# Kernel tuning notes

Measured on AMD Instinct MI355X. Metric: run time of the kernel, lower is better.

Reference implementation:

```python
import jax, jax.numpy as jnp
import numpy as np

N = 65536   # base nodes
M = 65536   # union local nodes
E = 1048576 # base edges
EL = 1048576 # local edges
K = 131072  # membership entries
F = 128     # in_channels
H = 128     # hidden_dim
L = 2       # num_layers
OUT = 2
ALPHA = 0.9


def setup_inputs() -> dict:
    key = jax.random.key(0)
    ks = jax.random.split(key, 16)
    s = 1.0 / np.sqrt(H)
    return {
        "x": jax.random.normal(ks[0], (N, F), jnp.float32),
        "edge_index": jax.random.randint(ks[1], (2, E), 0, N, jnp.int64 if jax.config.jax_enable_x64 else jnp.int32),
        "edge_weight": jax.random.uniform(ks[2], (E,), jnp.float32),
        "local_x0": jax.random.normal(ks[3], (M, F), jnp.float32),
        "copy2orig": jax.random.randint(ks[4], (M,), 0, N),
        "local_adj_index": jax.random.randint(ks[5], (2, EL), 0, M),
        "local_adj_value": jax.random.uniform(ks[6], (EL,), jnp.float32),
        "memb_idx": jax.random.randint(ks[7], (K,), 0, M),
        "memb_gid": jax.random.randint(ks[8], (K,), 0, 64),
        "B": 64,
        "Wb_in": jax.random.normal(ks[9], (F, H), jnp.float32) * s,
        "bb_in": jnp.zeros((H,), jnp.float32),
        "Wl_in": jax.random.normal(ks[10], (F, H), jnp.float32) * s,
        "bl_in": jnp.zeros((H,), jnp.float32),
        "W_base": jax.random.normal(ks[11], (L, H, H), jnp.float32) * s,
        "b_base": jnp.zeros((L, H), jnp.float32),
        "W_local": jax.random.normal(ks[12], (L, H, H), jnp.float32) * s,
        "b_local": jnp.zeros((L, H), jnp.float32),
        "Wp": jax.random.normal(ks[13], (H, OUT), jnp.float32) * s,
        "bp": jnp.zeros((OUT,), jnp.float32),
    }


def reference(x, edge_index, edge_weight, local_x0, copy2orig, local_adj_index,
              local_adj_value, memb_idx, memb_gid, B, Wb_in, bb_in, Wl_in, bl_in,
              W_base, b_base, W_local, b_local, Wp, bp):
    n = x.shape[0]
    m = local_x0.shape[0]
    # input projections (dropout is identity in eval mode)
    base_x = jax.nn.relu(x @ Wb_in + bb_in)
    local_x = jax.nn.relu(local_x0 @ Wl_in + bl_in)
    src, dst = edge_index[0], edge_index[1]
    lsrc, ldst = local_adj_index[0], local_adj_index[1]
    for l in range(W_base.shape[0]):
        # base graph propagation: normalized-adjacency spmm then linear+relu
        base_agg = jax.ops.segment_sum(base_x[src] * edge_weight[:, None], dst, num_segments=n)
        base_x = jax.nn.relu(base_agg @ W_base[l] + b_base[l])
        # local union-graph propagation + alpha-mix with base features via copy2orig
        local_agg = jax.ops.segment_sum(local_x[lsrc] * local_adj_value[:, None], ldst, num_segments=m)
        mix = ALPHA * local_agg + (1.0 - ALPHA) * base_x[copy2orig]
        local_x = jax.nn.relu(mix @ W_local[l] + b_local[l])
    # scatter-mean pooling by membership (fused sum + count)
    sub = jax.ops.segment_sum(local_x[memb_idx], memb_gid, num_segments=B)
    cnt = jax.ops.segment_sum(jnp.ones((memb_gid.shape[0], 1), local_x.dtype), memb_gid, num_segments=B)
    sub = sub / jnp.maximum(cnt, 1.0)
    return sub @ Wp + bp
```

## Files before the change

kernel.cpp:

```cpp
#include <hip/hip_runtime.h>

typedef __attribute__((ext_vector_type(8))) short bfrag;
typedef __attribute__((ext_vector_type(4))) float ffrag;

__device__ __forceinline__ ushort f2bf(float f) {
    union { float f; unsigned u; } v{f};
    unsigned r = v.u + 0x7fff + ((v.u >> 16) & 1);
    return (ushort)(r >> 16);
}
__device__ __forceinline__ float bf2f(ushort u) {
    union { unsigned u; float f; } v{(unsigned)u << 16};
    return v.f;
}
__device__ __forceinline__ float bflo(unsigned u) {
    union { unsigned u; float f; } v{u << 16};
    return v.f;
}
__device__ __forceinline__ float bfhi(unsigned u) {
    union { unsigned u; float f; } v{u & 0xffff0000u};
    return v.f;
}


__global__ __launch_bounds__(256) void zero_kernel(int* __restrict__ p, int n) {
    int i = blockIdx.x * 256 + threadIdx.x;
    if (i < n) p[i] = 0;
}


__global__ __launch_bounds__(256) void bhist(const int* __restrict__ dst, int* __restrict__ bcount) {
    __shared__ int h[256];
    const int t = threadIdx.x;
    h[t] = 0;
    __syncthreads();
    const int base = blockIdx.x * 4096;
#pragma unroll
    for (int u = 0; u < 16; ++u)
        atomicAdd(&h[((unsigned)dst[base + u * 256 + t]) >> 8], 1);
    __syncthreads();
    atomicAdd(&bcount[t], h[t]);
}

__global__ __launch_bounds__(256) void bscan(const int* __restrict__ bcount, int* __restrict__ bstart,
                                             int* __restrict__ bcursor) {
    __shared__ int s[256];
    const int t = threadIdx.x;
    int c = bcount[t];
    s[t] = c;
    __syncthreads();
    for (int o = 1; o < 256; o <<= 1) {
        int add = (t >= o) ? s[t - o] : 0;
        __syncthreads();
        s[t] += add;
        __syncthreads();
    }
    int excl = s[t] - c;
    bstart[t] = excl;
    bcursor[t] = excl;
    if (t == 255) bstart[256] = s[t];
}

#define CH 4096

__global__ __launch_bounds__(256) void bucket1(const int* __restrict__ src, const int* __restrict__ dst,
                                               const float* __restrict__ w, int* __restrict__ bcursor,
                                               int2* __restrict__ staged) {
    __shared__ int cnt_s[256], base_l[256], base_g[256], cur[256];
    __shared__ int2 stage[CH];
    __shared__ unsigned char bb[CH];
    const int t = threadIdx.x;
    const int base = blockIdx.x * CH;
    cnt_s[t] = 0;
    __syncthreads();
#pragma unroll
    for (int u = 0; u < CH / 256; ++u) {
        int b = ((unsigned)dst[base + u * 256 + t]) >> 8;
        atomicAdd(&cnt_s[b], 1);
    }
    __syncthreads();
    int v = cnt_s[t];
    base_l[t] = v;
    __syncthreads();
    for (int o = 1; o < 256; o <<= 1) {
        int add = (t >= o) ? base_l[t - o] : 0;
        __syncthreads();
        base_l[t] += add;
        __syncthreads();
    }
    int excl = base_l[t] - v;
    base_l[t] = excl;
    cur[t] = excl;
    base_g[t] = atomicAdd(&bcursor[t], v);
    __syncthreads();
#pragma unroll
    for (int u = 0; u < CH / 256; ++u) {
        int e = base + u * 256 + t;
        int d = dst[e];
        int b = ((unsigned)d) >> 8;
        int p = atomicAdd(&cur[b], 1);
        stage[p] = make_int2((src[e] & 0xffff) | ((d & 255) << 16), __float_as_int(w[e]));
        bb[p] = (unsigned char)b;
    }
    __syncthreads();
    for (int i = t; i < CH; i += 256) {
        int b = bb[i];
        staged[base_g[b] + (i - base_l[b])] = stage[i];
    }
}

__global__ __launch_bounds__(256) void bucket2n(const int* __restrict__ bstart, const int2* __restrict__ staged,
                                                int* __restrict__ start, int2* __restrict__ edges) {
    __shared__ int cnt[256], excl[256], cur[256];
    const int t = threadIdx.x;
    const int b = blockIdx.x;
    cnt[t] = 0;
    __syncthreads();
    const int s0 = bstart[b];
    const int s1 = bstart[b + 1];
    for (int i = s0 + t; i < s1; i += 256) {
        int dl = (staged[i].x >> 16) & 0xff;
        atomicAdd(&cnt[dl], 1);
    }
    __syncthreads();
    int v = cnt[t];
    excl[t] = v;
    __syncthreads();
    for (int o = 1; o < 256; o <<= 1) {
        int add = (t >= o) ? excl[t - o] : 0;
        __syncthreads();
        excl[t] += add;
        __syncthreads();
    }
    int e = excl[t] - v;
    cur[t] = e;
    start[b * 256 + t] = s0 + e;
    if (b == 255 && t == 255) start[256 * 256] = s1;
    __syncthreads();
    for (int i = s0 + t; i < s1; i += 256) {
        int2 se = staged[i];
        int dl = (se.x >> 16) & 0xff;
        int p = s0 + atomicAdd(&cur[dl], 1);
        edges[p] = make_int2(se.x & 0xffff, se.y);
    }
}


__global__ __launch_bounds__(256) void wprep(const float* __restrict__ Wb_in, const float* __restrict__ Wl_in,
                                             const float* __restrict__ W_base, const float* __restrict__ W_local,
                                             ushort* __restrict__ out) {
    int idx = blockIdx.x * 256 + threadIdx.x;
    int mat = idx >> 14;
    int i = idx & 16383;
    int nn = i >> 7, kk = i & 127;
    const float* src;
    switch (mat) {
        case 0: src = Wb_in; break;
        case 1: src = Wl_in; break;
        case 2: src = W_base; break;
        case 3: src = W_base + 16384; break;
        case 4: src = W_local; break;
        default: src = W_local + 16384; break;
    }
    out[(size_t)mat * 16384 + i] = f2bf(src[kk * 128 + nn]);
}


#define ASTRIDE 136

template <bool A_F32, bool MIX>
__global__ __launch_bounds__(256) void gemm_mfma(const void* __restrict__ Ap, const ushort* __restrict__ A2,
                                                 const int* __restrict__ ridx,
                                                 const ushort* __restrict__ Wt, const float* __restrict__ bias,
                                                 ushort* __restrict__ Y) {
    __shared__ ushort As[64 * ASTRIDE];
    __shared__ ushort Bs[128 * ASTRIDE];
    const int tid = threadIdx.x;
    const int r0 = blockIdx.x * 64;

    if (A_F32) {
        const float* A = (const float*)Ap;
#pragma unroll
        for (int p = 0; p < 8; ++p) {
            int c = p * 256 + tid;
            int row = c >> 5, o4 = (c & 31) * 4;
            float4 v = *(const float4*)(A + (size_t)(r0 + row) * 128 + o4);
            ushort4 u;
            u.x = f2bf(v.x); u.y = f2bf(v.y); u.z = f2bf(v.z); u.w = f2bf(v.w);
            *(ushort4*)&As[row * ASTRIDE + o4] = u;
        }
    } else {
        const ushort* A = (const ushort*)Ap;
#pragma unroll
        for (int p = 0; p < 4; ++p) {
            int c = p * 256 + tid;
            int row = c >> 4, o8 = (c & 15) * 8;
            uint4 v = *(const uint4*)(A + (size_t)(r0 + row) * 128 + o8);
            if (MIX) {
                int rr = ridx[r0 + row];
                uint4 v2 = *(const uint4*)(A2 + (size_t)rr * 128 + o8);
                uint4 o;
                float x0, x1;
                x0 = 0.9f * bflo(v.x) + 0.1f * bflo(v2.x);
                x1 = 0.9f * bfhi(v.x) + 0.1f * bfhi(v2.x);
                o.x = (unsigned)f2bf(x0) | ((unsigned)f2bf(x1) << 16);
                x0 = 0.9f * bflo(v.y) + 0.1f * bflo(v2.y);
                x1 = 0.9f * bfhi(v.y) + 0.1f * bfhi(v2.y);
                o.y = (unsigned)f2bf(x0) | ((unsigned)f2bf(x1) << 16);
                x0 = 0.9f * bflo(v.z) + 0.1f * bflo(v2.z);
                x1 = 0.9f * bfhi(v.z) + 0.1f * bfhi(v2.z);
                o.z = (unsigned)f2bf(x0) | ((unsigned)f2bf(x1) << 16);
                x0 = 0.9f * bflo(v.w) + 0.1f * bflo(v2.w);
                x1 = 0.9f * bfhi(v.w) + 0.1f * bfhi(v2.w);
                o.w = (unsigned)f2bf(x0) | ((unsigned)f2bf(x1) << 16);
                v = o;
            }
            *(uint4*)&As[row * ASTRIDE + o8] = v;
        }
    }
#pragma unroll
    for (int p = 0; p < 8; ++p) {
        int c = p * 256 + tid;
        int n = c >> 4, o8 = (c & 15) * 8;
        *(uint4*)&Bs[n * ASTRIDE + o8] = *(const uint4*)(Wt + n * 128 + o8);
    }
    __syncthreads();

    const int lane = tid & 63;
    const int w = tid >> 6;
    const int wm = (w & 1) * 32;
    const int wn = (w >> 1) * 64;
    const int q = lane >> 4;
    const int l16 = lane & 15;

    ffrag acc[2][4];
#pragma unroll
    for (int mt = 0; mt < 2; ++mt)
#pragma unroll
        for (int nt = 0; nt < 4; ++nt) acc[mt][nt] = (ffrag){0.f, 0.f, 0.f, 0.f};

#pragma unroll
    for (int kc = 0; kc < 4; ++kc) {
        bfrag a[2], b[4];
#pragma unroll
        for (int mt = 0; mt < 2; ++mt)
            a[mt] = *(const bfrag*)&As[(wm + mt * 16 + l16) * ASTRIDE + kc * 32 + q * 8];
#pragma unroll
        for (int nt = 0; nt < 4; ++nt)
            b[nt] = *(const bfrag*)&Bs[(wn + nt * 16 + l16) * ASTRIDE + kc * 32 + q * 8];
#pragma unroll
        for (int mt = 0; mt < 2; ++mt)
#pragma unroll
            for (int nt = 0; nt < 4; ++nt)
                acc[mt][nt] = __builtin_amdgcn_mfma_f32_16x16x32_bf16(a[mt], b[nt], acc[mt][nt], 0, 0, 0);
    }

    float bias_v[4];
#pragma unroll
    for (int nt = 0; nt < 4; ++nt) bias_v[nt] = bias[wn + nt * 16 + l16];
#pragma unroll
    for (int mt = 0; mt < 2; ++mt)
#pragma unroll
        for (int nt = 0; nt < 4; ++nt)
#pragma unroll
            for (int r = 0; r < 4; ++r) {
                int row = r0 + wm + mt * 16 + q * 4 + r;
                int col = wn + nt * 16 + l16;
                float v = fmaxf(acc[mt][nt][r] + bias_v[nt], 0.f);
                Y[(size_t)row * 128 + col] = f2bf(v);
            }
}


__global__ __launch_bounds__(256) void spmm_bf16(const int* __restrict__ start, const int2* __restrict__ edges,
                                                 const ushort* __restrict__ X, ushort* __restrict__ Y, int n) {
    int node = (blockIdx.x * 256 + threadIdx.x) >> 5;
    int lane = threadIdx.x & 31;
    if (node >= n) return;
    int s0 = start[node];
    int s1 = start[node + 1];
    const int f = lane * 4;
    float a0 = 0.f, a1 = 0.f, a2 = 0.f, a3 = 0.f;
    int e = s0;
    for (; e + 4 <= s1; e += 4) {
        int2 e0 = edges[e + 0], e1 = edges[e + 1], e2 = edges[e + 2], e3 = edges[e + 3];
        float w0 = __int_as_float(e0.y), w1 = __int_as_float(e1.y);
        float w2 = __int_as_float(e2.y), w3 = __int_as_float(e3.y);
        ushort4 v0 = *(const ushort4*)(X + (size_t)e0.x * 128 + f);
        ushort4 v1 = *(const ushort4*)(X + (size_t)e1.x * 128 + f);
        ushort4 v2 = *(const ushort4*)(X + (size_t)e2.x * 128 + f);
        ushort4 v3 = *(const ushort4*)(X + (size_t)e3.x * 128 + f);
        a0 += w0 * bf2f(v0.x) + w1 * bf2f(v1.x) + w2 * bf2f(v2.x) + w3 * bf2f(v3.x);
        a1 += w0 * bf2f(v0.y) + w1 * bf2f(v1.y) + w2 * bf2f(v2.y) + w3 * bf2f(v3.y);
        a2 += w0 * bf2f(v0.z) + w1 * bf2f(v1.z) + w2 * bf2f(v2.z) + w3 * bf2f(v3.z);
        a3 += w0 * bf2f(v0.w) + w1 * bf2f(v1.w) + w2 * bf2f(v2.w) + w3 * bf2f(v3.w);
    }
    for (; e < s1; ++e) {
        int2 ee = edges[e];
        float w = __int_as_float(ee.y);
        ushort4 v = *(const ushort4*)(X + (size_t)ee.x * 128 + f);
        a0 += w * bf2f(v.x);
        a1 += w * bf2f(v.y);
        a2 += w * bf2f(v.z);
        a3 += w * bf2f(v.w);
    }
    ushort4 o;
    o.x = f2bf(a0);
    o.y = f2bf(a1);
    o.z = f2bf(a2);
    o.w = f2bf(a3);
    *(ushort4*)(Y + (size_t)node * 128 + f) = o;
}


__global__ __launch_bounds__(256) void pool_hist(const int* __restrict__ memb_gid, int* __restrict__ gcount) {
    __shared__ int h[64];
    int t = threadIdx.x;
    if (t < 64) h[t] = 0;
    __syncthreads();
    int base = blockIdx.x * 1024;
#pragma unroll
    for (int u = 0; u < 4; ++u) atomicAdd(&h[memb_gid[base + u * 256 + t]], 1);
    __syncthreads();
    if (t < 64) atomicAdd(&gcount[t], h[t]);
}

__global__ __launch_bounds__(64) void pool_scan(const int* __restrict__ gcount, int* __restrict__ gstart,
                                                int* __restrict__ cursor) {
    __shared__ int s[64];
    int t = threadIdx.x;
    int c = gcount[t];
    s[t] = c;
    __syncthreads();
    int acc = 0;
    for (int j = 0; j < 64; ++j)
        if (j < t) acc += s[j];
    gstart[t] = acc;
    cursor[t] = acc;
    if (t == 63) gstart[64] = acc + c;
}

__global__ __launch_bounds__(256) void pool_scatter(const int* __restrict__ memb_idx,
                                                    const int* __restrict__ memb_gid,
                                                    int* __restrict__ cursor, int* __restrict__ sorted_idx) {
    __shared__ int lhist[64];
    __shared__ int lbase[64];
    __shared__ int loff[1024];
    int t = threadIdx.x;
    if (t < 64) lhist[t] = 0;
    __syncthreads();
    int base = blockIdx.x * 1024;
    int g[4], ix[4];
#pragma unroll
    for (int u = 0; u < 4; ++u) {
        int e = base + u * 256 + t;
        g[u] = memb_gid[e];
        ix[u] = memb_idx[e];
        loff[u * 256 + t] = atomicAdd(&lhist[g[u]], 1);
    }
    __syncthreads();
    if (t < 64) lbase[t] = atomicAdd(&cursor[t], lhist[t]);
    __syncthreads();
#pragma unroll
    for (int u = 0; u < 4; ++u) {
        int pos = lbase[g[u]] + loff[u * 256 + t];
        sorted_idx[pos] = ix[u];
    }
}

__global__ __launch_bounds__(256) void pool_accum(const int* __restrict__ gstart, const int* __restrict__ sorted_idx,
                                                  const ushort* __restrict__ X, float* __restrict__ gsum) {
    const int g = blockIdx.x >> 5;
    const int sgm = blockIdx.x & 31;
    const int gs = gstart[g];
    const int cnt = gstart[g + 1] - gs;
    const int e_begin = gs + ((cnt * sgm) >> 5);
    const int e_end = gs + ((cnt * (sgm + 1)) >> 5);
    const int t = threadIdx.x;
    const int fp = t & 63;
    const int sub = t >> 6;
    float ax = 0.f, ay = 0.f;
#pragma unroll 4
    for (int e = e_begin + sub; e < e_end; e += 4) {
        int idx = sorted_idx[e];
        ushort2 u = *(const ushort2*)(X + (size_t)idx * 128 + fp * 2);
        ax += bf2f(u.x);
        ay += bf2f(u.y);
    }
    __shared__ float sx[256], sy[256];
    sx[t] = ax;
    sy[t] = ay;
    __syncthreads();
    if (t < 64) {
        atomicAdd(&gsum[g * 128 + fp * 2 + 0], sx[t] + sx[t + 64] + sx[t + 128] + sx[t + 192]);
        atomicAdd(&gsum[g * 128 + fp * 2 + 1], sy[t] + sy[t + 64] + sy[t + 128] + sy[t + 192]);
    }
}


__global__ __launch_bounds__(128) void final_kernel(const float* __restrict__ gsum, const int* __restrict__ gcnt,
                                                    const float* __restrict__ Wp, const float* __restrict__ bp,
                                                    float* __restrict__ out) {
    int t = threadIdx.x;
    int g = t >> 1;
    int o = t & 1;
    float inv = 1.f / fmaxf((float)gcnt[g], 1.f);
    float acc = bp[o];
    for (int f = 0; f < 128; ++f) acc += gsum[g * 128 + f] * inv * Wp[f * 2 + o];
    out[g * 2 + o] = acc;
}


extern "C" void kernel_launch(void* const* d_in, const int* in_sizes, int n_in,
                              void* d_out, int out_size, void* d_ws, size_t ws_size,
                              hipStream_t stream) {
    const float* x              = (const float*)d_in[0];
    const int*   edge_index     = (const int*)d_in[1];
    const float* edge_weight    = (const float*)d_in[2];
    const float* local_x0       = (const float*)d_in[3];
    const int*   copy2orig      = (const int*)d_in[4];
    const int*   local_adj_idx  = (const int*)d_in[5];
    const float* local_adj_val  = (const float*)d_in[6];
    const int*   memb_idx       = (const int*)d_in[7];
    const int*   memb_gid       = (const int*)d_in[8];
    const float* Wb_in          = (const float*)d_in[10];
    const float* bb_in          = (const float*)d_in[11];
    const float* Wl_in          = (const float*)d_in[12];
    const float* bl_in          = (const float*)d_in[13];
    const float* W_base         = (const float*)d_in[14];
    const float* b_base         = (const float*)d_in[15];
    const float* W_local        = (const float*)d_in[16];
    const float* b_local        = (const float*)d_in[17];
    const float* Wp             = (const float*)d_in[18];
    const float* bp             = (const float*)d_in[19];
    float* out = (float*)d_out;

    constexpr int N = 65536, M = 65536, E = 1048576, EL = 1048576, K = 131072, H = 128;

    char* wsb = (char*)d_ws;
    size_t off = 0;
    auto alloc = [&](size_t bytes) -> char* {
        char* p = wsb + off;
        off += (bytes + 255) & ~(size_t)255;
        return p;
    };
    int*    bs_start = (int*)alloc((size_t)(N + 1) * 4);
    int2*   bs_edges = (int2*)alloc((size_t)E * 8);
    int2*   bs_stage = (int2*)alloc((size_t)E * 8);
    int*    bs_bcnt  = (int*)alloc(256 * 4);
    int*    bs_bsta  = (int*)alloc(257 * 4);
    int*    bs_bcur  = (int*)alloc(256 * 4);
    int*    ls_start = (int*)alloc((size_t)(M + 1) * 4);
    int2*   ls_edges = (int2*)alloc((size_t)EL * 8);
    int2*   ls_stage = (int2*)alloc((size_t)EL * 8);
    int*    ls_bcnt  = (int*)alloc(256 * 4);
    int*    ls_bsta  = (int*)alloc(257 * 4);
    int*    ls_bcur  = (int*)alloc(256 * 4);
    ushort* bufA     = (ushort*)alloc((size_t)N * H * 2);
    ushort* bufB     = (ushort*)alloc((size_t)M * H * 2);
    ushort* bufC     = (ushort*)alloc((size_t)N * H * 2);
    ushort* bufD     = (ushort*)alloc((size_t)M * H * 2);
    ushort* wt       = (ushort*)alloc((size_t)6 * 16384 * 2);
    int*    p_gcnt   = (int*)alloc(64 * 4);
    int*    p_gstart = (int*)alloc(65 * 4);
    int*    p_cursor = (int*)alloc(64 * 4);
    int*    p_sorted = (int*)alloc((size_t)K * 4);
    float*  pool_sum = (float*)alloc(64 * 128 * 4);

    const int* b_src = edge_index;
    const int* b_dst = edge_index + E;
    const int* l_src = local_adj_idx;
    const int* l_dst = local_adj_idx + EL;

    zero_kernel<<<1, 256, 0, stream>>>(bs_bcnt, 256);
    zero_kernel<<<1, 256, 0, stream>>>(ls_bcnt, 256);
    zero_kernel<<<1, 256, 0, stream>>>(p_gcnt, 64);
    zero_kernel<<<32, 256, 0, stream>>>((int*)pool_sum, 64 * 128);

    wprep<<<384, 256, 0, stream>>>(Wb_in, Wl_in, W_base, W_local, wt);

    bhist<<<E / 4096, 256, 0, stream>>>(b_dst, bs_bcnt);
    bscan<<<1, 256, 0, stream>>>(bs_bcnt, bs_bsta, bs_bcur);
    bucket1<<<E / CH, 256, 0, stream>>>(b_src, b_dst, edge_weight, bs_bcur, bs_stage);
    bucket2n<<<256, 256, 0, stream>>>(bs_bsta, bs_stage, bs_start, bs_edges);

    bhist<<<EL / 4096, 256, 0, stream>>>(l_dst, ls_bcnt);
    bscan<<<1, 256, 0, stream>>>(ls_bcnt, ls_bsta, ls_bcur);
    bucket1<<<EL / CH, 256, 0, stream>>>(l_src, l_dst, local_adj_val, ls_bcur, ls_stage);
    bucket2n<<<256, 256, 0, stream>>>(ls_bsta, ls_stage, ls_start, ls_edges);

    pool_hist<<<K / 1024, 256, 0, stream>>>(memb_gid, p_gcnt);
    pool_scan<<<1, 64, 0, stream>>>(p_gcnt, p_gstart, p_cursor);
    pool_scatter<<<K / 1024, 256, 0, stream>>>(memb_idx, memb_gid, p_cursor, p_sorted);

    gemm_mfma<true, false><<<N / 64, 256, 0, stream>>>(x, nullptr, nullptr, wt, bb_in, bufA);
    gemm_mfma<true, false><<<M / 64, 256, 0, stream>>>(local_x0, nullptr, nullptr, wt + 16384, bl_in, bufB);

    for (int l = 0; l < 2; ++l) {
        spmm_bf16<<<N * 32 / 256, 256, 0, stream>>>(bs_start, bs_edges, bufA, bufC, N);
        spmm_bf16<<<M * 32 / 256, 256, 0, stream>>>(ls_start, ls_edges, bufB, bufD, M);
        gemm_mfma<false, false><<<N / 64, 256, 0, stream>>>(bufC, nullptr, nullptr,
                                                            wt + (size_t)(2 + l) * 16384, b_base + (size_t)l * H, bufA);
        gemm_mfma<false, true><<<M / 64, 256, 0, stream>>>(bufD, bufA, copy2orig,
                                                           wt + (size_t)(4 + l) * 16384, b_local + (size_t)l * H, bufB);
    }

    pool_accum<<<64 * 32, 256, 0, stream>>>(p_gstart, p_sorted, bufB, pool_sum);
    final_kernel<<<1, 128, 0, stream>>>(pool_sum, p_gcnt, Wp, bp, out);
}
```

Baseline: 481.6 us.

## Fuse SpMM aggregation and alpha-mix into the MFMA GEMM prologue

Each SpMM is merged with the following linear layer: a block of 64 nodes aggregates its neighbours straight into shared memory, applies the alpha-mix with the base features in fp32, and then runs the MFMA GEMM. This removes the bufC/bufD round trip through global memory and half the kernel launches. Weight fragments are now read directly from global memory instead of being staged in shared memory, which cuts LDS use and raises occupancy but may cost L2 bandwidth. The mix is now applied before bf16 rounding, which changes numerics slightly.

Result: slower. 528.6 us (+9.8%).

```diff
diff --git a/kernel.cpp b/kernel.cpp
--- a/kernel.cpp
+++ b/kernel.cpp
@@ -10,14 +10,6 @@
 }
 __device__ __forceinline__ float bf2f(ushort u) {
     union { unsigned u; float f; } v{(unsigned)u << 16};
-    return v.f;
-}
-__device__ __forceinline__ float bflo(unsigned u) {
-    union { unsigned u; float f; } v{u << 16};
-    return v.f;
-}
-__device__ __forceinline__ float bfhi(unsigned u) {
-    union { unsigned u; float f; } v{u & 0xffff0000u};
     return v.f;
 }
 
@@ -164,64 +156,23 @@
     out[(size_t)mat * 16384 + i] = f2bf(src[kk * 128 + nn]);
 }
 
-
 #define ASTRIDE 136
 
-template <bool A_F32, bool MIX>
-__global__ __launch_bounds__(256) void gemm_mfma(const void* __restrict__ Ap, const ushort* __restrict__ A2,
-                                                 const int* __restrict__ ridx,
-                                                 const ushort* __restrict__ Wt, const float* __restrict__ bias,
-                                                 ushort* __restrict__ Y) {
+
+__global__ __launch_bounds__(256) void gemm_in(const float* __restrict__ A, const ushort* __restrict__ Wt,
+                                               const float* __restrict__ bias, ushort* __restrict__ Y) {
     __shared__ ushort As[64 * ASTRIDE];
-    __shared__ ushort Bs[128 * ASTRIDE];
     const int tid = threadIdx.x;
     const int r0 = blockIdx.x * 64;
 
-    if (A_F32) {
-        const float* A = (const float*)Ap;
-#pragma unroll
-        for (int p = 0; p < 8; ++p) {
-            int c = p * 256 + tid;
-            int row = c >> 5, o4 = (c & 31) * 4;
-            float4 v = *(const float4*)(A + (size_t)(r0 + row) * 128 + o4);
-            ushort4 u;
-            u.x = f2bf(v.x); u.y = f2bf(v.y); u.z = f2bf(v.z); u.w = f2bf(v.w);
-            *(ushort4*)&As[row * ASTRIDE + o4] = u;
-        }
-    } else {
-        const ushort* A = (const ushort*)Ap;
-#pragma unroll
-        for (int p = 0; p < 4; ++p) {
-            int c = p * 256 + tid;
-            int row = c >> 4, o8 = (c & 15) * 8;
-            uint4 v = *(const uint4*)(A + (size_t)(r0 + row) * 128 + o8);
-            if (MIX) {
-                int rr = ridx[r0 + row];
-                uint4 v2 = *(const uint4*)(A2 + (size_t)rr * 128 + o8);
-                uint4 o;
-                float x0, x1;
-                x0 = 0.9f * bflo(v.x) + 0.1f * bflo(v2.x);
-                x1 = 0.9f * bfhi(v.x) + 0.1f * bfhi(v2.x);
-                o.x = (unsigned)f2bf(x0) | ((unsigned)f2bf(x1) << 16);
-                x0 = 0.9f * bflo(v.y) + 0.1f * bflo(v2.y);
-                x1 = 0.9f * bfhi(v.y) + 0.1f * bfhi(v2.y);
-                o.y = (unsigned)f2bf(x0) | ((unsigned)f2bf(x1) << 16);
-                x0 = 0.9f * bflo(v.z) + 0.1f * bflo(v2.z);
-                x1 = 0.9f * bfhi(v.z) + 0.1f * bfhi(v2.z);
-                o.z = (unsigned)f2bf(x0) | ((unsigned)f2bf(x1) << 16);
-                x0 = 0.9f * bflo(v.w) + 0.1f * bflo(v2.w);
-                x1 = 0.9f * bfhi(v.w) + 0.1f * bfhi(v2.w);
-                o.w = (unsigned)f2bf(x0) | ((unsigned)f2bf(x1) << 16);
-                v = o;
-            }
-            *(uint4*)&As[row * ASTRIDE + o8] = v;
-        }
-    }
 #pragma unroll
     for (int p = 0; p < 8; ++p) {
         int c = p * 256 + tid;
-        int n = c >> 4, o8 = (c & 15) * 8;
-        *(uint4*)&Bs[n * ASTRIDE + o8] = *(const uint4*)(Wt + n * 128 + o8);
+        int row = c >> 5, o4 = (c & 31) * 4;
+        float4 v = *(const float4*)(A + (size_t)(r0 + row) * 128 + o4);
+        ushort4 u;
+        u.x = f2bf(v.x); u.y = f2bf(v.y); u.z = f2bf(v.z); u.w = f2bf(v.w);
+        *(ushort4*)&As[row * ASTRIDE + o4] = u;
     }
     __syncthreads();
 
@@ -246,7 +197,7 @@
             a[mt] = *(const bfrag*)&As[(wm + mt * 16 + l16) * ASTRIDE + kc * 32 + q * 8];
 #pragma unroll
         for (int nt = 0; nt < 4; ++nt)
-            b[nt] = *(const bfrag*)&Bs[(wn + nt * 16 + l16) * ASTRIDE + kc * 32 + q * 8];
+            b[nt] = *(const bfrag*)(Wt + (wn + nt * 16 + l16) * 128 + kc * 32 + q * 8);
 #pragma unroll
         for (int mt = 0; mt < 2; ++mt)
 #pragma unroll
@@ -271,44 +222,108 @@
 }
 
 
-__global__ __launch_bounds__(256) void spmm_bf16(const int* __restrict__ start, const int2* __restrict__ edges,
-                                                 const ushort* __restrict__ X, ushort* __restrict__ Y, int n) {
-    int node = (blockIdx.x * 256 + threadIdx.x) >> 5;
-    int lane = threadIdx.x & 31;
-    if (node >= n) return;
-    int s0 = start[node];
-    int s1 = start[node + 1];
+template <bool MIX>
+__global__ __launch_bounds__(256) void spmm_gemm(const int* __restrict__ start, const int2* __restrict__ edges,
+                                                 const ushort* __restrict__ X, const ushort* __restrict__ A2,
+                                                 const int* __restrict__ ridx, const ushort* __restrict__ Wt,
+                                                 const float* __restrict__ bias, ushort* __restrict__ Y) {
+    __shared__ ushort As[64 * ASTRIDE];
+    const int tid = threadIdx.x;
+    const int r0 = blockIdx.x * 64;
+    const int sw = tid >> 5;
+    const int lane = tid & 31;
     const int f = lane * 4;
-    float a0 = 0.f, a1 = 0.f, a2 = 0.f, a3 = 0.f;
-    int e = s0;
-    for (; e + 4 <= s1; e += 4) {
-        int2 e0 = edges[e + 0], e1 = edges[e + 1], e2 = edges[e + 2], e3 = edges[e + 3];
-        float w0 = __int_as_float(e0.y), w1 = __int_as_float(e1.y);
-        float w2 = __int_as_float(e2.y), w3 = __int_as_float(e3.y);
-        ushort4 v0 = *(const ushort4*)(X + (size_t)e0.x * 128 + f);
-        ushort4 v1 = *(const ushort4*)(X + (size_t)e1.x * 128 + f);
-        ushort4 v2 = *(const ushort4*)(X + (size_t)e2.x * 128 + f);
-        ushort4 v3 = *(const ushort4*)(X + (size_t)e3.x * 128 + f);
-        a0 += w0 * bf2f(v0.x) + w1 * bf2f(v1.x) + w2 * bf2f(v2.x) + w3 * bf2f(v3.x);
-        a1 += w0 * bf2f(v0.y) + w1 * bf2f(v1.y) + w2 * bf2f(v2.y) + w3 * bf2f(v3.y);
-        a2 += w0 * bf2f(v0.z) + w1 * bf2f(v1.z) + w2 * bf2f(v2.z) + w3 * bf2f(v3.z);
-        a3 += w0 * bf2f(v0.w) + w1 * bf2f(v1.w) + w2 * bf2f(v2.w) + w3 * bf2f(v3.w);
-    }
-    for (; e < s1; ++e) {
-        int2 ee = edges[e];
-        float w = __int_as_float(ee.y);
-        ushort4 v = *(const ushort4*)(X + (size_t)ee.x * 128 + f);
-        a0 += w * bf2f(v.x);
-        a1 += w * bf2f(v.y);
-        a2 += w * bf2f(v.z);
-        a3 += w * bf2f(v.w);
-    }
-    ushort4 o;
-    o.x = f2bf(a0);
-    o.y = f2bf(a1);
-    o.z = f2bf(a2);
-    o.w = f2bf(a3);
-    *(ushort4*)(Y + (size_t)node * 128 + f) = o;
+
+#pragma unroll
+    for (int i = 0; i < 8; ++i) {
+        const int node = r0 + i * 8 + sw;
+        const int rl = i * 8 + sw;
+        int s0 = start[node];
+        int s1 = start[node + 1];
+        float a0 = 0.f, a1 = 0.f, a2 = 0.f, a3 = 0.f;
+        int e = s0;
+        for (; e + 4 <= s1; e += 4) {
+            int2 e0 = edges[e + 0], e1 = edges[e + 1], e2 = edges[e + 2], e3 = edges[e + 3];
+            float w0 = __int_as_float(e0.y), w1 = __int_as_float(e1.y);
+            float w2 = __int_as_float(e2.y), w3 = __int_as_float(e3.y);
+            ushort4 v0 = *(const ushort4*)(X + (size_t)e0.x * 128 + f);
+            ushort4 v1 = *(const ushort4*)(X + (size_t)e1.x * 128 + f);
+            ushort4 v2 = *(const ushort4*)(X + (size_t)e2.x * 128 + f);
+            ushort4 v3 = *(const ushort4*)(X + (size_t)e3.x * 128 + f);
+            a0 += w0 * bf2f(v0.x) + w1 * bf2f(v1.x) + w2 * bf2f(v2.x) + w3 * bf2f(v3.x);
+            a1 += w0 * bf2f(v0.y) + w1 * bf2f(v1.y) + w2 * bf2f(v2.y) + w3 * bf2f(v3.y);
+            a2 += w0 * bf2f(v0.z) + w1 * bf2f(v1.z) + w2 * bf2f(v2.z) + w3 * bf2f(v3.z);
+            a3 += w0 * bf2f(v0.w) + w1 * bf2f(v1.w) + w2 * bf2f(v2.w) + w3 * bf2f(v3.w);
+        }
+        for (; e < s1; ++e) {
+            int2 ee = edges[e];
+            float w = __int_as_float(ee.y);
+            ushort4 v = *(const ushort4*)(X + (size_t)ee.x * 128 + f);
+            a0 += w * bf2f(v.x);
+            a1 += w * bf2f(v.y);
+            a2 += w * bf2f(v.z);
+            a3 += w * bf2f(v.w);
+        }
+        if (MIX) {
+            int rr = ridx[node];
+            ushort4 m = *(const ushort4*)(A2 + (size_t)rr * 128 + f);
+            a0 = 0.9f * a0 + 0.1f * bf2f(m.x);
+            a1 = 0.9f * a1 + 0.1f * bf2f(m.y);
+            a2 = 0.9f * a2 + 0.1f * bf2f(m.z);
+            a3 = 0.9f * a3 + 0.1f * bf2f(m.w);
+        }
+        ushort4 o;
+        o.x = f2bf(a0);
+        o.y = f2bf(a1);
+        o.z = f2bf(a2);
+        o.w = f2bf(a3);
+        *(ushort4*)&As[rl * ASTRIDE + f] = o;
+    }
+    __syncthreads();
+
+    const int wlane = tid & 63;
+    const int w = tid >> 6;
+    const int wm = (w & 1) * 32;
+    const int wn = (w >> 1) * 64;
+    const int q = wlane >> 4;
+    const int l16 = wlane & 15;
+
+    ffrag acc[2][4];
+#pragma unroll
+    for (int mt = 0; mt < 2; ++mt)
+#pragma unroll
+        for (int nt = 0; nt < 4; ++nt) acc[mt][nt] = (ffrag){0.f, 0.f, 0.f, 0.f};
+
+#pragma unroll
+    for (int kc = 0; kc < 4; ++kc) {
+        bfrag a[2], b[4];
+#pragma unroll
+        for (int mt = 0; mt < 2; ++mt)
+            a[mt] = *(const bfrag*)&As[(wm + mt * 16 + l16) * ASTRIDE + kc * 32 + q * 8];
+#pragma unroll
+        for (int nt = 0; nt < 4; ++nt)
+            b[nt] = *(const bfrag*)(Wt + (wn + nt * 16 + l16) * 128 + kc * 32 + q * 8);
+#pragma unroll
+        for (int mt = 0; mt < 2; ++mt)
+#pragma unroll
+            for (int nt = 0; nt < 4; ++nt)
+                acc[mt][nt] = __builtin_amdgcn_mfma_f32_16x16x32_bf16(a[mt], b[nt], acc[mt][nt], 0, 0, 0);
+    }
+
+    float bias_v[4];
+#pragma unroll
+    for (int nt = 0; nt < 4; ++nt) bias_v[nt] = bias[wn + nt * 16 + l16];
+#pragma unroll
+    for (int mt = 0; mt < 2; ++mt)
+#pragma unroll
+        for (int nt = 0; nt < 4; ++nt)
+#pragma unroll
+            for (int r = 0; r < 4; ++r) {
+                int row = r0 + wm + mt * 16 + q * 4 + r;
+                int col = wn + nt * 16 + l16;
+                float v = fmaxf(acc[mt][nt][r] + bias_v[nt], 0.f);
+                Y[(size_t)row * 128 + col] = f2bf(v);
+            }
 }
 
 
@@ -492,17 +507,17 @@
     pool_scan<<<1, 64, 0, stream>>>(p_gcnt, p_gstart, p_cursor);
     pool_scatter<<<K / 1024, 256, 0, stream>>>(memb_idx, memb_gid, p_cursor, p_sorted);
 
-    gemm_mfma<true, false><<<N / 64, 256, 0, stream>>>(x, nullptr, nullptr, wt, bb_in, bufA);
-    gemm_mfma<true, false><<<M / 64, 256, 0, stream>>>(local_x0, nullptr, nullptr, wt + 16384, bl_in, bufB);
-
-    for (int l = 0; l < 2; ++l) {
-        spmm_bf16<<<N * 32 / 256, 256, 0, stream>>>(bs_start, bs_edges, bufA, bufC, N);
-        spmm_bf16<<<M * 32 / 256, 256, 0, stream>>>(ls_start, ls_edges, bufB, bufD, M);
-        gemm_mfma<false, false><<<N / 64, 256, 0, stream>>>(bufC, nullptr, nullptr,
-                                                            wt + (size_t)(2 + l) * 16384, b_base + (size_t)l * H, bufA);
-        gemm_mfma<false, true><<<M / 64, 256, 0, stream>>>(bufD, bufA, copy2orig,
-                                                           wt + (size_t)(4 + l) * 16384, b_local + (size_t)l * H, bufB);
-    }
+    gemm_in<<<N / 64, 256, 0, stream>>>(x, wt, bb_in, bufA);
+    gemm_in<<<M / 64, 256, 0, stream>>>(local_x0, wt + 16384, bl_in, bufB);
+
+    spmm_gemm<false><<<N / 64, 256, 0, stream>>>(bs_start, bs_edges, bufA, nullptr, nullptr,
+                                                 wt + 2 * 16384, b_base, bufC);
+    spmm_gemm<true><<<M / 64, 256, 0, stream>>>(ls_start, ls_edges, bufB, bufC, copy2orig,
+                                                wt + 4 * 16384, b_local, bufD);
+    spmm_gemm<false><<<N / 64, 256, 0, stream>>>(bs_start, bs_edges, bufC, nullptr, nullptr,
+                                                 wt + 3 * 16384, b_base + H, bufA);
+    spmm_gemm<true><<<M / 64, 256, 0, stream>>>(ls_start, ls_edges, bufD, bufA, copy2orig,
+                                                wt + 5 * 16384, b_local + H, bufB);
 
     pool_accum<<<64 * 32, 256, 0, stream>>>(p_gstart, p_sorted, bufB, pool_sum);
     final_kernel<<<1, 128, 0, stream>>>(pool_sum, p_gcnt, Wp, bp, out);
```
